# Kernel tuning notes

Measured on AMD Instinct MI355X. Metric: run time of the kernel, lower is better.

The kernel has to match this reference:

```python
import jax, jax.numpy as jnp
import numpy as np

N_NODES = 100000
N_EDGES = 1600000
IN_FEAT = 64
HIDDEN = 64


def setup_inputs() -> dict:
    key = jax.random.key(0)
    ks = jax.random.split(key, 8)
    s = 0.05
    x = jax.random.normal(ks[0], (N_NODES, IN_FEAT), dtype=jnp.float32)
    edge_index = jax.random.randint(ks[1], (2, N_EDGES), 0, N_NODES, dtype=jnp.int64)
    return {
        "x": x,
        "edge_index": edge_index,
        "W_l1": jax.random.normal(ks[2], (HIDDEN, IN_FEAT), dtype=jnp.float32) * s,
        "b1": jnp.zeros((HIDDEN,), dtype=jnp.float32),
        "W_r1": jax.random.normal(ks[3], (HIDDEN, IN_FEAT), dtype=jnp.float32) * s,
        "W_l2": jax.random.normal(ks[4], (HIDDEN, HIDDEN), dtype=jnp.float32) * s,
        "b2": jnp.zeros((HIDDEN,), dtype=jnp.float32),
        "W_r2": jax.random.normal(ks[5], (HIDDEN, HIDDEN), dtype=jnp.float32) * s,
    }


def _sage_conv(h, src, dst, W_l, b, W_r):
    # PyG SAGEConv, aggr='mean': out_i = W_l @ mean_{j in N(i)} h_j + b + W_r @ h_i
    n = h.shape[0]
    msg = h[src]                                            # [E, d] gather
    agg = jax.ops.segment_sum(msg, dst, num_segments=n)     # [N, d] scatter-add
    cnt = jax.ops.segment_sum(jnp.ones((src.shape[0],), h.dtype), dst, num_segments=n)
    mean = agg / jnp.maximum(cnt, 1.0)[:, None]             # isolated nodes -> 0
    return mean @ W_l.T + b + h @ W_r.T


def reference(x, edge_index, W_l1, b1, W_r1, W_l2, b2, W_r2):
    src, dst = edge_index[0], edge_index[1]
    h = jax.nn.relu(_sage_conv(x, src, dst, W_l1, b1, W_r1))
    # dropout p=0.0 -> identity (eval mode)
    return jax.nn.relu(_sage_conv(h, src, dst, W_l2, b2, W_r2))
```

## Files before the change

### kernel.cpp

```cpp
#include <hip/hip_runtime.h>
#include <stdint.h>

#define N_NODES 100000
#define FEAT 64
#define SCAN_B 1024
#define BKT 256
#define NBINS ((N_NODES + BKT - 1) / BKT)
#define NTILES 256
#define SRC_MASK 0x00FFFFFFu

typedef __attribute__((ext_vector_type(8))) short bf16x8;
typedef __attribute__((ext_vector_type(4))) float f32x4;

__device__ __forceinline__ unsigned short f2bf(float f) {
    unsigned int u = __float_as_uint(f);
    u += 0x7fffu + ((u >> 16) & 1u);
    return (unsigned short)(u >> 16);
}

__global__ __launch_bounds__(256) void cvt_bf16_kernel(
    const float* __restrict__ in, unsigned short* __restrict__ out, int n8) {
    int i = blockIdx.x * blockDim.x + threadIdx.x;
    if (i >= n8) return;
    float4 a = ((const float4*)in)[i * 2];
    float4 b = ((const float4*)in)[i * 2 + 1];
    uint4 r;
    r.x = (unsigned int)f2bf(a.x) | ((unsigned int)f2bf(a.y) << 16);
    r.y = (unsigned int)f2bf(a.z) | ((unsigned int)f2bf(a.w) << 16);
    r.z = (unsigned int)f2bf(b.x) | ((unsigned int)f2bf(b.y) << 16);
    r.w = (unsigned int)f2bf(b.z) | ((unsigned int)f2bf(b.w) << 16);
    ((uint4*)out)[i] = r;
}


__global__ __launch_bounds__(256) void tile_hist_kernel(
    const int* __restrict__ dst, int* __restrict__ H, int nE, int tileEdges) {
    __shared__ int hist[NBINS];
    const int tile = blockIdx.x;
    const int tid = threadIdx.x;
    for (int i = tid; i < NBINS; i += 256) hist[i] = 0;
    __syncthreads();
    int e0 = tile * tileEdges;
    int e1 = min(e0 + tileEdges, nE);
    for (int e = e0 + tid; e < e1; e += 256) atomicAdd(&hist[dst[e] >> 8], 1);
    __syncthreads();
    for (int i = tid; i < NBINS; i += 256) H[i * NTILES + tile] = hist[i];
}

__global__ __launch_bounds__(SCAN_B) void scan1_kernel(
    const int* __restrict__ deg, int* __restrict__ P,
    int* __restrict__ bsum, int n) {
    __shared__ int tmp[SCAN_B];
    int t = threadIdx.x;
    int gid = blockIdx.x * SCAN_B + t;
    int v = (gid < n) ? deg[gid] : 0;
    tmp[t] = v;
    __syncthreads();
    for (int off = 1; off < SCAN_B; off <<= 1) {
        int a = (t >= off) ? tmp[t - off] : 0;
        __syncthreads();
        tmp[t] += a;
        __syncthreads();
    }
    if (gid < n) P[gid] = tmp[t] - v;
    if (t == SCAN_B - 1) bsum[blockIdx.x] = tmp[t];
}

__global__ __launch_bounds__(128) void scan2_kernel(int* __restrict__ bsum, int nb) {
    __shared__ int tmp[128];
    int t = threadIdx.x;
    int v = (t < nb) ? bsum[t] : 0;
    tmp[t] = v;
    __syncthreads();
    for (int off = 1; off < 128; off <<= 1) {
        int a = (t >= off) ? tmp[t - off] : 0;
        __syncthreads();
        tmp[t] += a;
        __syncthreads();
    }
    if (t < nb) bsum[t] = tmp[t] - v;
}

__global__ __launch_bounds__(256) void scan3_kernel(
    int* __restrict__ P, const int* __restrict__ bsum, int n, int total) {
    int gid = blockIdx.x * blockDim.x + threadIdx.x;
    if (gid < n) P[gid] += bsum[gid >> 10];
    if (gid == 0) P[n] = total;
}

__global__ __launch_bounds__(256) void scatter_bucket_kernel(
    const int* __restrict__ src, const int* __restrict__ dst,
    const int* __restrict__ P, unsigned int* __restrict__ packed,
    int nE, int tileEdges) {
    __shared__ int cur[NBINS];
    const int tile = blockIdx.x;
    const int tid = threadIdx.x;
    for (int i = tid; i < NBINS; i += 256) cur[i] = P[i * NTILES + tile];
    __syncthreads();
    int e0 = tile * tileEdges;
    int e1 = min(e0 + tileEdges, nE);
    for (int e = e0 + tid; e < e1; e += 256) {
        int d = dst[e];
        int pos = atomicAdd(&cur[d >> 8], 1);
        packed[pos] = ((unsigned int)(d & (BKT - 1)) << 24) | (unsigned int)src[e];
    }
}

__global__ __launch_bounds__(256) void bucket_sort_kernel(
    const unsigned int* __restrict__ packed,
    const int* __restrict__ P,
    int* __restrict__ rowptr,
    int* __restrict__ ssrc,
    int nE) {
    __shared__ int hist[BKT];
    __shared__ int cur[BKT];
    const int b = blockIdx.x;
    const int tid = threadIdx.x;

    hist[tid] = 0;
    __syncthreads();
    const int start = P[b * NTILES];
    const int end = (b + 1 < NBINS) ? P[(b + 1) * NTILES] : nE;
    for (int j = start + tid; j < end; j += 256)
        atomicAdd(&hist[packed[j] >> 24], 1);
    __syncthreads();

    int v = hist[tid];
    for (int off = 1; off < 256; off <<= 1) {
        int a = (tid >= off) ? hist[tid - off] : 0;
        __syncthreads();
        hist[tid] += a;
        __syncthreads();
    }
    int excl = hist[tid] - v;

    int node = b * BKT + tid;
    if (node <= N_NODES) rowptr[node] = start + excl;
    cur[tid] = start + excl;
    __syncthreads();

    for (int j = start + tid; j < end; j += 256) {
        unsigned int p = packed[j];
        int pos = atomicAdd(&cur[p >> 24], 1);
        ssrc[pos] = (int)(p & SRC_MASK);
    }
}

__global__ __launch_bounds__(256) void agg_bf16_kernel(
    const unsigned short* __restrict__ featb,
    const int* __restrict__ rowptr,
    const int* __restrict__ ssrc,
    unsigned short* __restrict__ meanb,
    int nNodes) {
    int tid = blockIdx.x * blockDim.x + threadIdx.x;
    int node = tid >> 3;
    if (node >= nNodes) return;
    int chunk = tid & 7;
    const uint4* feat16 = (const uint4*)featb;

    int beg = rowptr[node];
    int end = rowptr[node + 1];
    float acc0 = 0.f, acc1 = 0.f, acc2 = 0.f, acc3 = 0.f;
    float acc4 = 0.f, acc5 = 0.f, acc6 = 0.f, acc7 = 0.f;

#define ADDROW(a)                                         \
    acc0 += __uint_as_float((a).x << 16);                 \
    acc1 += __uint_as_float((a).x & 0xffff0000u);         \
    acc2 += __uint_as_float((a).y << 16);                 \
    acc3 += __uint_as_float((a).y & 0xffff0000u);         \
    acc4 += __uint_as_float((a).z << 16);                 \
    acc5 += __uint_as_float((a).z & 0xffff0000u);         \
    acc6 += __uint_as_float((a).w << 16);                 \
    acc7 += __uint_as_float((a).w & 0xffff0000u);

    int j = beg;
    for (; j + 4 <= end; j += 4) {
        int s0 = ssrc[j + 0];
        int s1 = ssrc[j + 1];
        int s2 = ssrc[j + 2];
        int s3 = ssrc[j + 3];
        uint4 a0 = feat16[(size_t)s0 * 8 + chunk];
        uint4 a1 = feat16[(size_t)s1 * 8 + chunk];
        uint4 a2 = feat16[(size_t)s2 * 8 + chunk];
        uint4 a3 = feat16[(size_t)s3 * 8 + chunk];
        ADDROW(a0) ADDROW(a1) ADDROW(a2) ADDROW(a3)
    }
    for (; j < end; ++j) {
        uint4 a = feat16[(size_t)ssrc[j] * 8 + chunk];
        ADDROW(a)
    }
#undef ADDROW

    int deg = end - beg;
    float inv = 1.0f / (float)(deg > 0 ? deg : 1);
    uint4 r;
    r.x = (unsigned int)f2bf(acc0 * inv) | ((unsigned int)f2bf(acc1 * inv) << 16);
    r.y = (unsigned int)f2bf(acc2 * inv) | ((unsigned int)f2bf(acc3 * inv) << 16);
    r.z = (unsigned int)f2bf(acc4 * inv) | ((unsigned int)f2bf(acc5 * inv) << 16);
    r.w = (unsigned int)f2bf(acc6 * inv) | ((unsigned int)f2bf(acc7 * inv) << 16);
    ((uint4*)meanb)[(size_t)node * 8 + chunk] = r;
}


__device__ __forceinline__ bf16x8 pack8(const float* __restrict__ p) {
    float4 a = *(const float4*)p;
    float4 b = *(const float4*)(p + 4);
    bf16x8 r;
    r[0] = (short)f2bf(a.x); r[1] = (short)f2bf(a.y);
    r[2] = (short)f2bf(a.z); r[3] = (short)f2bf(a.w);
    r[4] = (short)f2bf(b.x); r[5] = (short)f2bf(b.y);
    r[6] = (short)f2bf(b.z); r[7] = (short)f2bf(b.w);
    return r;
}

template <bool OUT_BF16>
__global__ __launch_bounds__(256) void mfma_linear_kernel(
    const unsigned short* __restrict__ meanb,
    const unsigned short* __restrict__ xb,
    const float* __restrict__ Wl,
    const float* __restrict__ bias,
    const float* __restrict__ Wr,
    void* __restrict__ outp,
    int nGroups) {
    const int lane = (int)(threadIdx.x & 63);
    const int col = lane & 15;
    const int kg = lane >> 4;

    bf16x8 bfr[4][4];
#pragma unroll
    for (int t = 0; t < 4; ++t) {
        const int n = t * 16 + col;
#pragma unroll
        for (int kk = 0; kk < 4; ++kk) {
            const float* w = (kk < 2 ? Wl : Wr) + n * 64 + (kk & 1) * 32 + kg * 8;
            bfr[t][kk] = pack8(w);
        }
    }
    float bv[4];
#pragma unroll
    for (int t = 0; t < 4; ++t) bv[t] = bias[t * 16 + col];

    const int wave = (int)((blockIdx.x * blockDim.x + threadIdx.x) >> 6);
    const int nWaves = (int)((gridDim.x * blockDim.x) >> 6);

    for (int g = wave; g < nGroups; g += nWaves) {
        const int arow = g * 16 + col;
        const unsigned short* mrow = meanb + (size_t)arow * FEAT + kg * 8;
        const unsigned short* xrow = xb + (size_t)arow * FEAT + kg * 8;

        f32x4 acc[4];
#pragma unroll
        for (int t = 0; t < 4; ++t) acc[t] = (f32x4){0.f, 0.f, 0.f, 0.f};

#pragma unroll
        for (int kk = 0; kk < 4; ++kk) {
            const unsigned short* p =
                (kk < 2) ? (mrow + (kk & 1) * 32) : (xrow + (kk & 1) * 32);
            bf16x8 a = *(const bf16x8*)p;
#pragma unroll
            for (int t = 0; t < 4; ++t)
                acc[t] = __builtin_amdgcn_mfma_f32_16x16x32_bf16(a, bfr[t][kk], acc[t], 0, 0, 0);
        }

#pragma unroll
        for (int t = 0; t < 4; ++t) {
#pragma unroll
            for (int r = 0; r < 4; ++r) {
                int node = g * 16 + kg * 4 + r;
                float v = fmaxf(acc[t][r] + bv[t], 0.0f);
                if (OUT_BF16)
                    ((unsigned short*)outp)[(size_t)node * FEAT + t * 16 + col] = f2bf(v);
                else
                    ((float*)outp)[(size_t)node * FEAT + t * 16 + col] = v;
            }
        }
    }
}

extern "C" void kernel_launch(void* const* d_in, const int* in_sizes, int n_in,
                              void* d_out, int out_size, void* d_ws, size_t ws_size,
                              hipStream_t stream) {
    const float* x   = (const float*)d_in[0];
    const int* ei    = (const int*)d_in[1];
    const float* Wl1 = (const float*)d_in[2];
    const float* b1  = (const float*)d_in[3];
    const float* Wr1 = (const float*)d_in[4];
    const float* Wl2 = (const float*)d_in[5];
    const float* b2  = (const float*)d_in[6];
    const float* Wr2 = (const float*)d_in[7];

    const int E = in_sizes[1] / 2;
    const int* src = ei;
    const int* dst = ei + E;
    const int N = N_NODES;

    const int n2 = NBINS * NTILES;
    const int TE = (E + NTILES - 1) / NTILES;
    const int NB2 = (n2 + SCAN_B - 1) / SCAN_B;

    int* H      = (int*)d_ws;
    int* P      = H + n2;
    int* bsum   = P + (n2 + 8);
    unsigned int* packed = (unsigned int*)(bsum + 128);
    int* rowptr = (int*)(packed + E);
    int* ssrc   = rowptr + (N + 8);
    unsigned short* meanb = (unsigned short*)(ssrc + E);
    unsigned short* xb    = meanb + (size_t)N * FEAT;
    unsigned short* hb    = xb + (size_t)N * FEAT;
    float* out  = (float*)d_out;

    const int NG = N / 16;

    cvt_bf16_kernel<<<(N * FEAT / 8 + 255) / 256, 256, 0, stream>>>(x, xb, N * FEAT / 8);
    tile_hist_kernel<<<NTILES, 256, 0, stream>>>(dst, H, E, TE);
    scan1_kernel<<<NB2, SCAN_B, 0, stream>>>(H, P, bsum, n2);
    scan2_kernel<<<1, 128, 0, stream>>>(bsum, NB2);
    scan3_kernel<<<(n2 + 256) / 256, 256, 0, stream>>>(P, bsum, n2, E);
    scatter_bucket_kernel<<<NTILES, 256, 0, stream>>>(src, dst, P, packed, E, TE);
    bucket_sort_kernel<<<NBINS, 256, 0, stream>>>(packed, P, rowptr, ssrc, E);

    agg_bf16_kernel<<<(N * 8 + 255) / 256, 256, 0, stream>>>(xb, rowptr, ssrc, meanb, N);
    mfma_linear_kernel<true><<<256, 256, 0, stream>>>(meanb, xb, Wl1, b1, Wr1, hb, NG);

    agg_bf16_kernel<<<(N * 8 + 255) / 256, 256, 0, stream>>>(hb, rowptr, ssrc, meanb, N);
    mfma_linear_kernel<false><<<256, 256, 0, stream>>>(meanb, hb, Wl2, b2, Wr2, out, NG);
}
```

Measured before the change: 183.0 us.

## Store bf16 features in chunk-sliced layout so aggregation gathers per slice

```diff
diff --git a/kernel.cpp b/kernel.cpp
--- a/kernel.cpp
+++ b/kernel.cpp
@@ -7,6 +7,7 @@
 #define BKT 256
 #define NBINS ((N_NODES + BKT - 1) / BKT)
 #define NTILES 256
+#define NSLICE 8
 #define SRC_MASK 0x00FFFFFFu
 
 typedef __attribute__((ext_vector_type(8))) short bf16x8;
@@ -18,18 +19,20 @@
     return (unsigned short)(u >> 16);
 }
 
-__global__ __launch_bounds__(256) void cvt_bf16_kernel(
-    const float* __restrict__ in, unsigned short* __restrict__ out, int n8) {
+__global__ __launch_bounds__(256) void cvt_bf16_sliced_kernel(
+    const float* __restrict__ in, uint4* __restrict__ out_cs, int n8) {
     int i = blockIdx.x * blockDim.x + threadIdx.x;
     if (i >= n8) return;
-    float4 a = ((const float4*)in)[i * 2];
-    float4 b = ((const float4*)in)[i * 2 + 1];
+    int node = i >> 3, c = i & 7;
+    const float4* p = (const float4*)(in + (size_t)node * FEAT + c * 8);
+    float4 a = p[0];
+    float4 b = p[1];
     uint4 r;
     r.x = (unsigned int)f2bf(a.x) | ((unsigned int)f2bf(a.y) << 16);
     r.y = (unsigned int)f2bf(a.z) | ((unsigned int)f2bf(a.w) << 16);
     r.z = (unsigned int)f2bf(b.x) | ((unsigned int)f2bf(b.y) << 16);
     r.w = (unsigned int)f2bf(b.z) | ((unsigned int)f2bf(b.w) << 16);
-    ((uint4*)out)[i] = r;
+    out_cs[(size_t)c * N_NODES + node] = r;
 }
 
 
@@ -146,17 +149,17 @@
     }
 }
 
-__global__ __launch_bounds__(256) void agg_bf16_kernel(
-    const unsigned short* __restrict__ featb,
+__global__ __launch_bounds__(256) void agg_sliced_kernel(
+    const uint4* __restrict__ feat_cs,
     const int* __restrict__ rowptr,
     const int* __restrict__ ssrc,
-    unsigned short* __restrict__ meanb,
+    uint4* __restrict__ mean_cs,
     int nNodes) {
-    int tid = blockIdx.x * blockDim.x + threadIdx.x;
-    int node = tid >> 3;
+    const int c = blockIdx.x & 7;
+    const int bin = blockIdx.x >> 3;
+    const int node = bin * BKT + threadIdx.x;
     if (node >= nNodes) return;
-    int chunk = tid & 7;
-    const uint4* feat16 = (const uint4*)featb;
+    const uint4* fs = feat_cs + (size_t)c * N_NODES;
 
     int beg = rowptr[node];
     int end = rowptr[node + 1];
@@ -179,14 +182,14 @@
         int s1 = ssrc[j + 1];
         int s2 = ssrc[j + 2];
         int s3 = ssrc[j + 3];
-        uint4 a0 = feat16[(size_t)s0 * 8 + chunk];
-        uint4 a1 = feat16[(size_t)s1 * 8 + chunk];
-        uint4 a2 = feat16[(size_t)s2 * 8 + chunk];
-        uint4 a3 = feat16[(size_t)s3 * 8 + chunk];
+        uint4 a0 = fs[s0];
+        uint4 a1 = fs[s1];
+        uint4 a2 = fs[s2];
+        uint4 a3 = fs[s3];
         ADDROW(a0) ADDROW(a1) ADDROW(a2) ADDROW(a3)
     }
     for (; j < end; ++j) {
-        uint4 a = feat16[(size_t)ssrc[j] * 8 + chunk];
+        uint4 a = fs[ssrc[j]];
         ADDROW(a)
     }
 #undef ADDROW
@@ -198,7 +201,7 @@
     r.y = (unsigned int)f2bf(acc2 * inv) | ((unsigned int)f2bf(acc3 * inv) << 16);
     r.z = (unsigned int)f2bf(acc4 * inv) | ((unsigned int)f2bf(acc5 * inv) << 16);
     r.w = (unsigned int)f2bf(acc6 * inv) | ((unsigned int)f2bf(acc7 * inv) << 16);
-    ((uint4*)meanb)[(size_t)node * 8 + chunk] = r;
+    mean_cs[(size_t)c * N_NODES + node] = r;
 }
 
 
@@ -215,8 +218,8 @@
 
 template <bool OUT_BF16>
 __global__ __launch_bounds__(256) void mfma_linear_kernel(
-    const unsigned short* __restrict__ meanb,
-    const unsigned short* __restrict__ xb,
+    const uint4* __restrict__ mean_cs,
+    const uint4* __restrict__ x_cs,
     const float* __restrict__ Wl,
     const float* __restrict__ bias,
     const float* __restrict__ Wr,
@@ -245,8 +248,6 @@
 
     for (int g = wave; g < nGroups; g += nWaves) {
         const int arow = g * 16 + col;
-        const unsigned short* mrow = meanb + (size_t)arow * FEAT + kg * 8;
-        const unsigned short* xrow = xb + (size_t)arow * FEAT + kg * 8;
 
         f32x4 acc[4];
 #pragma unroll
@@ -254,9 +255,10 @@
 
 #pragma unroll
         for (int kk = 0; kk < 4; ++kk) {
-            const unsigned short* p =
-                (kk < 2) ? (mrow + (kk & 1) * 32) : (xrow + (kk & 1) * 32);
-            bf16x8 a = *(const bf16x8*)p;
+            const int s = (kk & 1) * 4 + kg;
+            const uint4* base = (kk < 2) ? mean_cs : x_cs;
+            uint4 av = base[(size_t)s * N_NODES + arow];
+            bf16x8 a = *(const bf16x8*)&av;
 #pragma unroll
             for (int t = 0; t < 4; ++t)
                 acc[t] = __builtin_amdgcn_mfma_f32_16x16x32_bf16(a, bfr[t][kk], acc[t], 0, 0, 0);
@@ -268,10 +270,13 @@
             for (int r = 0; r < 4; ++r) {
                 int node = g * 16 + kg * 4 + r;
                 float v = fmaxf(acc[t][r] + bv[t], 0.0f);
-                if (OUT_BF16)
-                    ((unsigned short*)outp)[(size_t)node * FEAT + t * 16 + col] = f2bf(v);
-                else
+                if (OUT_BF16) {
+                    int f = t * 16 + col;
+                    int slice = f >> 3;
+                    ((unsigned short*)outp)[((size_t)slice * N_NODES + node) * 8 + (f & 7)] = f2bf(v);
+                } else {
                     ((float*)outp)[(size_t)node * FEAT + t * 16 + col] = v;
+                }
             }
         }
     }
@@ -304,14 +309,14 @@
     unsigned int* packed = (unsigned int*)(bsum + 128);
     int* rowptr = (int*)(packed + E);
     int* ssrc   = rowptr + (N + 8);
-    unsigned short* meanb = (unsigned short*)(ssrc + E);
-    unsigned short* xb    = meanb + (size_t)N * FEAT;
-    unsigned short* hb    = xb + (size_t)N * FEAT;
+    uint4* mean_cs = (uint4*)(ssrc + E);
+    uint4* x_cs    = mean_cs + (size_t)NSLICE * N;
+    uint4* h_cs    = x_cs + (size_t)NSLICE * N;
     float* out  = (float*)d_out;
 
     const int NG = N / 16;
 
-    cvt_bf16_kernel<<<(N * FEAT / 8 + 255) / 256, 256, 0, stream>>>(x, xb, N * FEAT / 8);
+    cvt_bf16_sliced_kernel<<<(N * 8 + 255) / 256, 256, 0, stream>>>(x, x_cs, N * 8);
     tile_hist_kernel<<<NTILES, 256, 0, stream>>>(dst, H, E, TE);
     scan1_kernel<<<NB2, SCAN_B, 0, stream>>>(H, P, bsum, n2);
     scan2_kernel<<<1, 128, 0, stream>>>(bsum, NB2);
@@ -319,9 +324,9 @@
     scatter_bucket_kernel<<<NTILES, 256, 0, stream>>>(src, dst, P, packed, E, TE);
     bucket_sort_kernel<<<NBINS, 256, 0, stream>>>(packed, P, rowptr, ssrc, E);
 
-    agg_bf16_kernel<<<(N * 8 + 255) / 256, 256, 0, stream>>>(xb, rowptr, ssrc, meanb, N);
-    mfma_linear_kernel<true><<<256, 256, 0, stream>>>(meanb, xb, Wl1, b1, Wr1, hb, NG);
-
-    agg_bf16_kernel<<<(N * 8 + 255) / 256, 256, 0, stream>>>(hb, rowptr, ssrc, meanb, N);
-    mfma_linear_kernel<false><<<256, 256, 0, stream>>>(meanb, hb, Wl2, b2, Wr2, out, NG);
-}
+    agg_sliced_kernel<<<NBINS * NSLICE, 256, 0, stream>>>(x_cs, rowptr, ssrc, mean_cs, N);
+    mfma_linear_kernel<true><<<256, 256, 0, stream>>>(mean_cs, x_cs, Wl1, b1, Wr1, h_cs, NG);
+
+    agg_sliced_kernel<<<NBINS * NSLICE, 256, 0, stream>>>(h_cs, rowptr, ssrc, mean_cs, N);
+    mfma_linear_kernel<false><<<256, 256, 0, stream>>>(mean_cs, h_cs, Wl2, b2, Wr2, out, NG);
+}
```

Result: slower. 224.8 us (+22.8%).

## Split neighbor aggregation into four source-range partitions with partial sums reduced in linear

Applied to the files above, without the earlier changes.

```diff
diff --git a/kernel.cpp b/kernel.cpp
--- a/kernel.cpp
+++ b/kernel.cpp
@@ -6,7 +6,9 @@
 #define SCAN_B 1024
 #define BKT 256
 #define NBINS ((N_NODES + BKT - 1) / BKT)
-#define NTILES 256
+#define NTILES 1024
+#define NRANGE 4
+#define RANGE_DIV 25000
 #define SRC_MASK 0x00FFFFFFu
 
 typedef __attribute__((ext_vector_type(8))) short bf16x8;
@@ -17,6 +19,8 @@
     u += 0x7fffu + ((u >> 16) & 1u);
     return (unsigned short)(u >> 16);
 }
+__device__ __forceinline__ float bflo(unsigned int u) { return __uint_as_float(u << 16); }
+__device__ __forceinline__ float bfhi(unsigned int u) { return __uint_as_float(u & 0xffff0000u); }
 
 __global__ __launch_bounds__(256) void cvt_bf16_kernel(
     const float* __restrict__ in, unsigned short* __restrict__ out, int n8) {
@@ -66,13 +70,13 @@
     if (t == SCAN_B - 1) bsum[blockIdx.x] = tmp[t];
 }
 
-__global__ __launch_bounds__(128) void scan2_kernel(int* __restrict__ bsum, int nb) {
-    __shared__ int tmp[128];
+__global__ __launch_bounds__(512) void scan2_kernel(int* __restrict__ bsum, int nb) {
+    __shared__ int tmp[512];
     int t = threadIdx.x;
     int v = (t < nb) ? bsum[t] : 0;
     tmp[t] = v;
     __syncthreads();
-    for (int off = 1; off < 128; off <<= 1) {
+    for (int off = 1; off < 512; off <<= 1) {
         int a = (t >= off) ? tmp[t - off] : 0;
         __syncthreads();
         tmp[t] += a;
@@ -109,96 +113,113 @@
 __global__ __launch_bounds__(256) void bucket_sort_kernel(
     const unsigned int* __restrict__ packed,
     const int* __restrict__ P,
-    int* __restrict__ rowptr,
+    int* __restrict__ rowptr2,
+    float* __restrict__ invdeg,
     int* __restrict__ ssrc,
     int nE) {
-    __shared__ int hist[BKT];
-    __shared__ int cur[BKT];
+    __shared__ int hist[BKT * NRANGE];
+    __shared__ int cur[BKT * NRANGE];
+    __shared__ int scanbuf[BKT];
     const int b = blockIdx.x;
-    const int tid = threadIdx.x;
-
-    hist[tid] = 0;
+    const int t = threadIdx.x;
+
+#pragma unroll
+    for (int i = 0; i < NRANGE; ++i) hist[t * NRANGE + i] = 0;
     __syncthreads();
     const int start = P[b * NTILES];
     const int end = (b + 1 < NBINS) ? P[(b + 1) * NTILES] : nE;
-    for (int j = start + tid; j < end; j += 256)
-        atomicAdd(&hist[packed[j] >> 24], 1);
-    __syncthreads();
-
-    int v = hist[tid];
+    for (int j = start + t; j < end; j += 256) {
+        unsigned int p = packed[j];
+        int s = (int)(p & SRC_MASK);
+        atomicAdd(&hist[(int)(p >> 24) * NRANGE + s / RANGE_DIV], 1);
+    }
+    __syncthreads();
+
+    int c0 = hist[t * NRANGE + 0], c1 = hist[t * NRANGE + 1];
+    int c2 = hist[t * NRANGE + 2], c3 = hist[t * NRANGE + 3];
+    int tot = c0 + c1 + c2 + c3;
+    int node = b * BKT + t;
+    if (node < N_NODES) invdeg[node] = 1.0f / (float)(tot > 0 ? tot : 1);
+    scanbuf[t] = tot;
+    __syncthreads();
     for (int off = 1; off < 256; off <<= 1) {
-        int a = (tid >= off) ? hist[tid - off] : 0;
-        __syncthreads();
-        hist[tid] += a;
-        __syncthreads();
-    }
-    int excl = hist[tid] - v;
-
-    int node = b * BKT + tid;
-    if (node <= N_NODES) rowptr[node] = start + excl;
-    cur[tid] = start + excl;
-    __syncthreads();
-
-    for (int j = start + tid; j < end; j += 256) {
+        int a = (t >= off) ? scanbuf[t - off] : 0;
+        __syncthreads();
+        scanbuf[t] += a;
+        __syncthreads();
+    }
+    int base = start + scanbuf[t] - tot;
+    int e0 = base, e1 = base + c0, e2 = e1 + c1, e3 = e2 + c2;
+    rowptr2[node * 4 + 0] = e0;
+    rowptr2[node * 4 + 1] = e1;
+    rowptr2[node * 4 + 2] = e2;
+    rowptr2[node * 4 + 3] = e3;
+    cur[t * NRANGE + 0] = e0;
+    cur[t * NRANGE + 1] = e1;
+    cur[t * NRANGE + 2] = e2;
+    cur[t * NRANGE + 3] = e3;
+    __syncthreads();
+
+    for (int j = start + t; j < end; j += 256) {
         unsigned int p = packed[j];
-        int pos = atomicAdd(&cur[p >> 24], 1);
-        ssrc[pos] = (int)(p & SRC_MASK);
-    }
-}
-
-__global__ __launch_bounds__(256) void agg_bf16_kernel(
+        int s = (int)(p & SRC_MASK);
+        int pos = atomicAdd(&cur[(int)(p >> 24) * NRANGE + s / RANGE_DIV], 1);
+        ssrc[pos] = s;
+    }
+}
+
+__global__ __launch_bounds__(256) void agg_part_kernel(
     const unsigned short* __restrict__ featb,
-    const int* __restrict__ rowptr,
+    const int* __restrict__ rowptr2,
     const int* __restrict__ ssrc,
-    unsigned short* __restrict__ meanb,
+    unsigned short* __restrict__ part,
     int nNodes) {
-    int tid = blockIdx.x * blockDim.x + threadIdx.x;
-    int node = tid >> 3;
-    if (node >= nNodes) return;
-    int chunk = tid & 7;
+    const int c = blockIdx.x & 3;
+    const int bin = blockIdx.x >> 2;
+    const int slot = threadIdx.x >> 3;
+    const int chunk = threadIdx.x & 7;
     const uint4* feat16 = (const uint4*)featb;
 
-    int beg = rowptr[node];
-    int end = rowptr[node + 1];
-    float acc0 = 0.f, acc1 = 0.f, acc2 = 0.f, acc3 = 0.f;
-    float acc4 = 0.f, acc5 = 0.f, acc6 = 0.f, acc7 = 0.f;
-
-#define ADDROW(a)                                         \
-    acc0 += __uint_as_float((a).x << 16);                 \
-    acc1 += __uint_as_float((a).x & 0xffff0000u);         \
-    acc2 += __uint_as_float((a).y << 16);                 \
-    acc3 += __uint_as_float((a).y & 0xffff0000u);         \
-    acc4 += __uint_as_float((a).z << 16);                 \
-    acc5 += __uint_as_float((a).z & 0xffff0000u);         \
-    acc6 += __uint_as_float((a).w << 16);                 \
-    acc7 += __uint_as_float((a).w & 0xffff0000u);
-
-    int j = beg;
-    for (; j + 4 <= end; j += 4) {
-        int s0 = ssrc[j + 0];
-        int s1 = ssrc[j + 1];
-        int s2 = ssrc[j + 2];
-        int s3 = ssrc[j + 3];
-        uint4 a0 = feat16[(size_t)s0 * 8 + chunk];
-        uint4 a1 = feat16[(size_t)s1 * 8 + chunk];
-        uint4 a2 = feat16[(size_t)s2 * 8 + chunk];
-        uint4 a3 = feat16[(size_t)s3 * 8 + chunk];
-        ADDROW(a0) ADDROW(a1) ADDROW(a2) ADDROW(a3)
-    }
-    for (; j < end; ++j) {
-        uint4 a = feat16[(size_t)ssrc[j] * 8 + chunk];
-        ADDROW(a)
-    }
+#pragma unroll
+    for (int g = 0; g < 8; ++g) {
+        int node = bin * BKT + g * 32 + slot;
+        if (node >= nNodes) continue;
+        int beg = rowptr2[node * 4 + c];
+        int end = rowptr2[node * 4 + c + 1];
+        float acc0 = 0.f, acc1 = 0.f, acc2 = 0.f, acc3 = 0.f;
+        float acc4 = 0.f, acc5 = 0.f, acc6 = 0.f, acc7 = 0.f;
+
+#define ADDROW(a)                                 \
+    acc0 += bflo((a).x); acc1 += bfhi((a).x);     \
+    acc2 += bflo((a).y); acc3 += bfhi((a).y);     \
+    acc4 += bflo((a).z); acc5 += bfhi((a).z);     \
+    acc6 += bflo((a).w); acc7 += bfhi((a).w);
+
+        int j = beg;
+        for (; j + 4 <= end; j += 4) {
+            int s0 = ssrc[j + 0];
+            int s1 = ssrc[j + 1];
+            int s2 = ssrc[j + 2];
+            int s3 = ssrc[j + 3];
+            uint4 a0 = feat16[(size_t)s0 * 8 + chunk];
+            uint4 a1 = feat16[(size_t)s1 * 8 + chunk];
+            uint4 a2 = feat16[(size_t)s2 * 8 + chunk];
+            uint4 a3 = feat16[(size_t)s3 * 8 + chunk];
+            ADDROW(a0) ADDROW(a1) ADDROW(a2) ADDROW(a3)
+        }
+        for (; j < end; ++j) {
+            uint4 a = feat16[(size_t)ssrc[j] * 8 + chunk];
+            ADDROW(a)
+        }
 #undef ADDROW
 
-    int deg = end - beg;
-    float inv = 1.0f / (float)(deg > 0 ? deg : 1);
-    uint4 r;
-    r.x = (unsigned int)f2bf(acc0 * inv) | ((unsigned int)f2bf(acc1 * inv) << 16);
-    r.y = (unsigned int)f2bf(acc2 * inv) | ((unsigned int)f2bf(acc3 * inv) << 16);
-    r.z = (unsigned int)f2bf(acc4 * inv) | ((unsigned int)f2bf(acc5 * inv) << 16);
-    r.w = (unsigned int)f2bf(acc6 * inv) | ((unsigned int)f2bf(acc7 * inv) << 16);
-    ((uint4*)meanb)[(size_t)node * 8 + chunk] = r;
+        uint4 r;
+        r.x = (unsigned int)f2bf(acc0) | ((unsigned int)f2bf(acc1) << 16);
+        r.y = (unsigned int)f2bf(acc2) | ((unsigned int)f2bf(acc3) << 16);
+        r.z = (unsigned int)f2bf(acc4) | ((unsigned int)f2bf(acc5) << 16);
+        r.w = (unsigned int)f2bf(acc6) | ((unsigned int)f2bf(acc7) << 16);
+        ((uint4*)part)[((size_t)c * N_NODES + node) * 8 + chunk] = r;
+    }
 }
 
 
@@ -215,7 +236,8 @@
 
 template <bool OUT_BF16>
 __global__ __launch_bounds__(256) void mfma_linear_kernel(
-    const unsigned short* __restrict__ meanb,
+    const unsigned short* __restrict__ part,
+    const float* __restrict__ invdeg,
     const unsigned short* __restrict__ xb,
     const float* __restrict__ Wl,
     const float* __restrict__ bias,
@@ -225,6 +247,7 @@
     const int lane = (int)(threadIdx.x & 63);
     const int col = lane & 15;
     const int kg = lane >> 4;
+    const uint4* part4 = (const uint4*)part;
 
     bf16x8 bfr[4][4];
 #pragma unroll
@@ -245,7 +268,7 @@
 
     for (int g = wave; g < nGroups; g += nWaves) {
         const int arow = g * 16 + col;
-        const unsigned short* mrow = meanb + (size_t)arow * FEAT + kg * 8;
+        const float invd = invdeg[arow];
         const unsigned short* xrow = xb + (size_t)arow * FEAT + kg * 8;
 
         f32x4 acc[4];
@@ -254,9 +277,28 @@
 
 #pragma unroll
         for (int kk = 0; kk < 4; ++kk) {
-            const unsigned short* p =
-                (kk < 2) ? (mrow + (kk & 1) * 32) : (xrow + (kk & 1) * 32);
-            bf16x8 a = *(const bf16x8*)p;
+            bf16x8 a;
+            if (kk < 2) {
+                const size_t u = (size_t)arow * 8 + (kk & 1) * 4 + kg;
+                uint4 q0 = part4[u];
+                uint4 q1 = part4[(size_t)1 * N_NODES * 8 + u];
+                uint4 q2 = part4[(size_t)2 * N_NODES * 8 + u];
+                uint4 q3 = part4[(size_t)3 * N_NODES * 8 + u];
+                float m0 = (bflo(q0.x) + bflo(q1.x)) + (bflo(q2.x) + bflo(q3.x));
+                float m1 = (bfhi(q0.x) + bfhi(q1.x)) + (bfhi(q2.x) + bfhi(q3.x));
+                float m2 = (bflo(q0.y) + bflo(q1.y)) + (bflo(q2.y) + bflo(q3.y));
+                float m3 = (bfhi(q0.y) + bfhi(q1.y)) + (bfhi(q2.y) + bfhi(q3.y));
+                float m4 = (bflo(q0.z) + bflo(q1.z)) + (bflo(q2.z) + bflo(q3.z));
+                float m5 = (bfhi(q0.z) + bfhi(q1.z)) + (bfhi(q2.z) + bfhi(q3.z));
+                float m6 = (bflo(q0.w) + bflo(q1.w)) + (bflo(q2.w) + bflo(q3.w));
+                float m7 = (bfhi(q0.w) + bfhi(q1.w)) + (bfhi(q2.w) + bfhi(q3.w));
+                a[0] = (short)f2bf(m0 * invd); a[1] = (short)f2bf(m1 * invd);
+                a[2] = (short)f2bf(m2 * invd); a[3] = (short)f2bf(m3 * invd);
+                a[4] = (short)f2bf(m4 * invd); a[5] = (short)f2bf(m5 * invd);
+                a[6] = (short)f2bf(m6 * invd); a[7] = (short)f2bf(m7 * invd);
+            } else {
+                a = *(const bf16x8*)(xrow + (kk & 1) * 32);
+            }
 #pragma unroll
             for (int t = 0; t < 4; ++t)
                 acc[t] = __builtin_amdgcn_mfma_f32_16x16x32_bf16(a, bfr[t][kk], acc[t], 0, 0, 0);
@@ -298,30 +340,31 @@
     const int TE = (E + NTILES - 1) / NTILES;
     const int NB2 = (n2 + SCAN_B - 1) / SCAN_B;
 
-    int* H      = (int*)d_ws;
-    int* P      = H + n2;
-    int* bsum   = P + (n2 + 8);
-    unsigned int* packed = (unsigned int*)(bsum + 128);
-    int* rowptr = (int*)(packed + E);
-    int* ssrc   = rowptr + (N + 8);
-    unsigned short* meanb = (unsigned short*)(ssrc + E);
-    unsigned short* xb    = meanb + (size_t)N * FEAT;
-    unsigned short* hb    = xb + (size_t)N * FEAT;
-    float* out  = (float*)d_out;
+    int* H        = (int*)d_ws;
+    int* P        = H + n2;
+    int* bsum     = P + (n2 + 8);
+    int* rowptr2  = bsum + 512;
+    float* invdeg = (float*)(rowptr2 + n2);
+    int* ssrc     = (int*)(invdeg + N);
+    unsigned short* xb = (unsigned short*)(ssrc + E);
+    unsigned short* hb = xb + (size_t)N * FEAT;
+    unsigned short* part = hb + (size_t)N * FEAT;
+    unsigned int* packed = (unsigned int*)part;
+    float* out = (float*)d_out;
 
     const int NG = N / 16;
 
     cvt_bf16_kernel<<<(N * FEAT / 8 + 255) / 256, 256, 0, stream>>>(x, xb, N * FEAT / 8);
     tile_hist_kernel<<<NTILES, 256, 0, stream>>>(dst, H, E, TE);
     scan1_kernel<<<NB2, SCAN_B, 0, stream>>>(H, P, bsum, n2);
-    scan2_kernel<<<1, 128, 0, stream>>>(bsum, NB2);
+    scan2_kernel<<<1, 512, 0, stream>>>(bsum, NB2);
     scan3_kernel<<<(n2 + 256) / 256, 256, 0, stream>>>(P, bsum, n2, E);
     scatter_bucket_kernel<<<NTILES, 256, 0, stream>>>(src, dst, P, packed, E, TE);
-    bucket_sort_kernel<<<NBINS, 256, 0, stream>>>(packed, P, rowptr, ssrc, E);
-
-    agg_bf16_kernel<<<(N * 8 + 255) / 256, 256, 0, stream>>>(xb, rowptr, ssrc, meanb, N);
-    mfma_linear_kernel<true><<<256, 256, 0, stream>>>(meanb, xb, Wl1, b1, Wr1, hb, NG);
-
-    agg_bf16_kernel<<<(N * 8 + 255) / 256, 256, 0, stream>>>(hb, rowptr, ssrc, meanb, N);
-    mfma_linear_kernel<false><<<256, 256, 0, stream>>>(meanb, hb, Wl2, b2, Wr2, out, NG);
-}
+    bucket_sort_kernel<<<NBINS, 256, 0, stream>>>(packed, P, rowptr2, invdeg, ssrc, E);
+
+    agg_part_kernel<<<NBINS * NRANGE, 256, 0, stream>>>(xb, rowptr2, ssrc, part, N);
+    mfma_linear_kernel<true><<<256, 256, 0, stream>>>(part, invdeg, xb, Wl1, b1, Wr1, hb, NG);
+
+    agg_part_kernel<<<NBINS * NRANGE, 256, 0, stream>>>(hb, rowptr2, ssrc, part, N);
+    mfma_linear_kernel<false><<<256, 256, 0, stream>>>(part, invdeg, hb, Wl2, b2, Wr2, out, NG);
+}
```

Measured after the change: 176.9 us. 1.03x faster.
